# Optimization experiments

Measured on AMD Instinct MI355X. Metric: run time of the kernel, lower is better.

## Reference

```python
import jax, jax.numpy as jnp
import numpy as np
from jax import lax

B, NQ, C = 2, 1024, 2048
H, DH = 16, 128
G, CD = 4, 512          # off_grps, off_dim = C // G
LR, HR = 24, 72         # low-res grid side, high-res grid side
INTER = 64
K = LR * LR             # sampled K/V tokens (grid_size == lr_size)


def setup_inputs() -> dict:
    key = jax.random.key(0)
    ks = jax.random.split(key, 16)
    s = 0.02
    d = {}
    d['hidden_states'] = jax.random.normal(ks[0], (B, NQ, C), jnp.float32)
    d['image_hd'] = jax.random.normal(ks[1], (B, HR * HR, C), jnp.float32)
    d['wq'] = jax.random.normal(ks[2], (C, C), jnp.float32) * s
    d['wk'] = jax.random.normal(ks[3], (C, C), jnp.float32) * s
    d['wv'] = jax.random.normal(ks[4], (C, C), jnp.float32) * s
    d['wo'] = jax.random.normal(ks[5], (C, C), jnp.float32) * s
    d['conv_dw_w'] = jax.random.normal(ks[6], (CD, 1, 3, 3), jnp.float32) * s
    d['ln1_w'] = jnp.ones((CD,), jnp.float32)
    d['ln1_b'] = jnp.zeros((CD,), jnp.float32)
    d['conv_lr_proj_w'] = jax.random.normal(ks[7], (INTER, CD), jnp.float32) * s
    d['proj_int_w'] = jax.random.normal(ks[8], (INTER, CD), jnp.float32) * s
    d['proj_int_b'] = jnp.zeros((INTER,), jnp.float32)
    d['ln2_w'] = jnp.ones((INTER,), jnp.float32)
    d['ln2_b'] = jnp.zeros((INTER,), jnp.float32)
    d['conv_off_w'] = jax.random.normal(ks[9], (2, INTER), jnp.float32) * s
    d['k_hd_w'] = jax.random.normal(ks[10], (C, C), jnp.float32) * s
    d['k_hd_b'] = jnp.zeros((C,), jnp.float32)
    d['v_hd_w'] = jax.random.normal(ks[11], (C, C), jnp.float32) * s
    d['v_hd_b'] = jnp.zeros((C,), jnp.float32)
    return d


def _ln_channels(x, w, b, eps=1e-5):
    # LayerNorm2d: normalize over channel axis of [N, C, H, W]
    mu = jnp.mean(x, axis=1, keepdims=True)
    var = jnp.var(x, axis=1, keepdims=True)
    xn = (x - mu) * lax.rsqrt(var + eps)
    return xn * w[None, :, None, None] + b[None, :, None, None]


def _tokens_to_grid(x, S):
    # [B, S*S, C] -> [B*G, CD, S, S]  (group channels like einops '(b) (h w) (g c) -> (b g) c h w')
    return x.reshape(B, S, S, G, CD).transpose(0, 3, 4, 1, 2).reshape(B * G, CD, S, S)


def _bilinear_sample(img, grid):
    # img [N, C, Hh, Wh]; grid [N, K, 2] (x, y) normalized to [-1, 1], align_corners=True
    N, Cc, Hh, Wh = img.shape
    x = (grid[..., 0] + 1.0) * 0.5 * (Wh - 1)
    y = (grid[..., 1] + 1.0) * 0.5 * (Hh - 1)
    x0f, y0f = jnp.floor(x), jnp.floor(y)
    wx = (x - x0f)[:, None, :]
    wy = (y - y0f)[:, None, :]
    x0 = jnp.clip(x0f.astype(jnp.int32), 0, Wh - 1)
    x1 = jnp.clip(x0 + 1, 0, Wh - 1)
    y0 = jnp.clip(y0f.astype(jnp.int32), 0, Hh - 1)
    y1 = jnp.clip(y0 + 1, 0, Hh - 1)
    imgf = img.reshape(N, Cc, Hh * Wh)
    gather = jax.vmap(lambda im, ix: im[:, ix])  # ([C,HW],[K]) -> [C,K]
    v00 = gather(imgf, y0 * Wh + x0)
    v01 = gather(imgf, y0 * Wh + x1)
    v10 = gather(imgf, y1 * Wh + x0)
    v11 = gather(imgf, y1 * Wh + x1)
    return (v00 * (1 - wx) * (1 - wy) + v01 * wx * (1 - wy)
            + v10 * (1 - wx) * wy + v11 * wx * wy)  # [N, C, K]


def _ref_grid():
    # normalized reference points as in _grid_generate (centers / (S-1) * 2 - 1)
    yy = (jnp.linspace(0.5, LR - 0.5, LR) / (LR - 1.0)) * 2.0 - 1.0
    xx = (jnp.linspace(0.5, LR - 0.5, LR) / (LR - 1.0)) * 2.0 - 1.0
    gy, gx = jnp.meshgrid(yy, xx, indexing='ij')
    return jnp.stack([gx, gy], axis=-1).reshape(K, 2)  # (x, y)


def reference(hidden_states, image_hd, wq, wk, wv, wo, conv_dw_w, ln1_w, ln1_b,
              conv_lr_proj_w, proj_int_w, proj_int_b, ln2_w, ln2_b, conv_off_w,
              k_hd_w, k_hd_b, v_hd_w, v_hd_b):
    # ---- QKV on the full sequence ----
    q = hidden_states @ wq.T
    k_txt = hidden_states @ wk.T
    v_txt = hidden_states @ wv.T

    # ---- offset network on LR image tokens (first LR*LR tokens) ----
    lr = _tokens_to_grid(hidden_states[:, :K, :], LR)          # [B*G, CD, LR, LR]
    x = lax.conv_general_dilated(lr, conv_dw_w, (1, 1), 'SAME',
                                 feature_group_count=CD,
                                 dimension_numbers=('NCHW', 'OIHW', 'NCHW'))
    x = jax.nn.silu(x)
    x = _ln_channels(x, ln1_w, ln1_b)
    x = jnp.einsum('nchw,oc->nohw', x, conv_lr_proj_w)          # 1x1 conv -> [B*G, INTER, LR, LR]
    # intention gate from spatially pooled group features
    pooled = jnp.mean(lr, axis=(2, 3))                          # [B*G, CD]
    gate = jax.nn.sigmoid(pooled @ proj_int_w.T + proj_int_b)   # [B*G, INTER]
    x = x * gate[:, :, None, None]
    x = _ln_channels(x, ln2_w, ln2_b)
    off = jnp.einsum('nchw,oc->nohw', x, conv_off_w)            # [B*G, 2, LR, LR]
    off = off.transpose(0, 2, 3, 1).reshape(B * G, K, 2)        # (x, y)
    pos = jnp.tanh(_ref_grid()[None] + off)                     # sampling locs in [-1, 1]

    # ---- deformable gather from HD features ----
    hd = _tokens_to_grid(image_hd, HR)                          # [B*G, CD, HR, HR]
    samp = _bilinear_sample(hd, pos)                            # [B*G, CD, K]
    samp = samp.reshape(B, G, CD, K).transpose(0, 3, 1, 2).reshape(B, K, C)
    k_hd = samp @ k_hd_w.T + k_hd_b
    v_hd = samp @ v_hd_w.T + v_hd_b

    # ---- attention: causal over text tokens, HD tokens fully visible ----
    k_all = jnp.concatenate([k_txt, k_hd], axis=1)              # [B, NQ+K, C]
    v_all = jnp.concatenate([v_txt, v_hd], axis=1)
    qh = q.reshape(B, NQ, H, DH).transpose(0, 2, 1, 3)
    kh = k_all.reshape(B, NQ + K, H, DH).transpose(0, 2, 1, 3)
    vh = v_all.reshape(B, NQ + K, H, DH).transpose(0, 2, 1, 3)
    scores = jnp.einsum('bhqd,bhkd->bhqk', qh, kh) / jnp.sqrt(jnp.float32(DH))
    col = jnp.arange(NQ + K)
    row = jnp.arange(NQ)
    allow = (col[None, :] >= NQ) | (col[None, :] <= row[:, None])
    scores = jnp.where(allow[None, None], scores, jnp.float32(-1e9))
    attn = jax.nn.softmax(scores, axis=-1)
    out = jnp.einsum('bhqk,bhkd->bhqd', attn, vh)
    out = out.transpose(0, 2, 1, 3).reshape(B, NQ, C)
    return out @ wo.T
```

## Files before the change

kernel.cpp:

```cpp
#include <hip/hip_runtime.h>

typedef unsigned short u16;
typedef unsigned int u32;
typedef __attribute__((ext_vector_type(8))) short bf8;
typedef __attribute__((ext_vector_type(4))) float f4;
typedef __attribute__((ext_vector_type(4))) unsigned short us4;

constexpr int B = 2;
constexpr int NQ = 1024;
constexpr int C = 2048;
constexpr int DH = 128;
constexpr int G = 4;
constexpr int CD = 512;
constexpr int LR = 24;
constexpr int HR = 72;
constexpr int INTER = 64;
constexpr int K = LR * LR;
constexpr int NKV = NQ + K;

#define MFMA16(a, b, c) __builtin_amdgcn_mfma_f32_16x16x32_bf16(a, b, c, 0, 0, 0)
#define GLDS(g, l)                                                         \
  __builtin_amdgcn_global_load_lds(                                        \
      (const __attribute__((address_space(1))) void*)(g),                  \
      (__attribute__((address_space(3))) void*)(l), 16, 0, 0)
#define SB()                               \
  do {                                     \
    __builtin_amdgcn_sched_barrier(0);     \
    __builtin_amdgcn_s_barrier();          \
    __builtin_amdgcn_sched_barrier(0);     \
  } while (0)
#define WVM(n)                                              \
  do {                                                      \
    asm volatile("s_waitcnt vmcnt(" #n ")" ::: "memory");   \
    __builtin_amdgcn_sched_barrier(0);                      \
  } while (0)

__device__ __forceinline__ u16 f2bf1(float f) {
  u32 u = __float_as_uint(f);
  u32 r = (u + 0x7fffu + ((u >> 16) & 1u)) >> 16;
  return (u16)r;
}

__global__ __launch_bounds__(256) void f2bf_k9b(
    const float* __restrict__ s0, const float* __restrict__ s1,
    const float* __restrict__ s2, const float* __restrict__ s3,
    const float* __restrict__ s4, const float* __restrict__ s5,
    const float* __restrict__ s6, const float* __restrict__ plrw,
    const float* __restrict__ cdw, u16* __restrict__ d0, u16* __restrict__ d1,
    u16* __restrict__ d2, u16* __restrict__ d3, u16* __restrict__ d4,
    u16* __restrict__ d5, u16* __restrict__ d6, float* __restrict__ wt,
    float* __restrict__ x1, float* __restrict__ pooled) {
  __shared__ float SH[16 * 577];
  const int y = blockIdx.y;
  const int t = threadIdx.x;
  if (y == 7) {
    if (blockIdx.x >= 128) return;
    const int idx = blockIdx.x * 256 + t;
    wt[idx] = plrw[(idx & 63) * 512 + (idx >> 6)];
    return;
  }
  if (y == 8) {
    if (blockIdx.x >= 256) return;
    const int n = blockIdx.x >> 5, cg = blockIdx.x & 31;
    const int b = n >> 2, g = n & 3;
    const int c0 = cg * 16;
    {
      const int c = t & 15, pr = t >> 4;
      const float* src = s0 + (size_t)b * 1024 * 2048 + g * 512 + c0 + c;
#pragma unroll 4
      for (int j = 0; j < 36; ++j) {
        const int p = j * 16 + pr;
        SH[c * 577 + p] = src[(size_t)p * 2048];
      }
    }
    __syncthreads();
    {
      const int c = t >> 4, seg = t & 15;
      float s = 0.f;
      for (int i = 0; i < 36; ++i) s += SH[c * 577 + seg * 36 + i];
      s += __shfl_xor(s, 1);
      s += __shfl_xor(s, 2);
      s += __shfl_xor(s, 4);
      s += __shfl_xor(s, 8);
      if (seg == 0) pooled[n * 512 + c0 + c] = s * (1.f / 576.f);
    }
    const size_t base_out = (size_t)(n * 512 + c0) * 576;
    for (int j = 0; j < 36; ++j) {
      const int idx = j * 256 + t;
      const int c = idx / 576, p = idx - c * 576;
      const int yy0 = p / 24, xx0 = p - yy0 * 24;
      const float* wp = cdw + (c0 + c) * 9;
      float s = 0.f;
#pragma unroll
      for (int dy = -1; dy <= 1; ++dy)
#pragma unroll
        for (int dx = -1; dx <= 1; ++dx) {
          const int yy = yy0 + dy, xx = xx0 + dx;
          if (yy < 0 || yy >= 24 || xx < 0 || xx >= 24) continue;
          s += SH[c * 577 + yy * 24 + xx] * wp[(dy + 1) * 3 + dx + 1];
        }
      x1[base_out + idx] = s / (1.f + expf(-s));
    }
    return;
  }
  const float* s;
  u16* d;
  switch (y) {
    case 0: s = s0; d = d0; break;
    case 1: s = s1; d = d1; break;
    case 2: s = s2; d = d2; break;
    case 3: s = s3; d = d3; break;
    case 4: s = s4; d = d4; break;
    case 5: s = s5; d = d5; break;
    default: s = s6; d = d6; break;
  }
  u16* L = (u16*)SH;
  const int pc = blockIdx.x;
  const int mb = pc >> 5, kb = pc & 31;
  const int rin = t >> 2, c0 = (t & 3) * 16;
  const float* src = s + (size_t)(mb * 64 + rin) * 2048 + kb * 64 + c0;
#pragma unroll
  for (int j = 0; j < 16; j += 4) {
    float4 v = *(const float4*)(src + j);
    L[rin * 68 + c0 + j] = f2bf1(v.x);
    L[rin * 68 + c0 + j + 1] = f2bf1(v.y);
    L[rin * 68 + c0 + j + 2] = f2bf1(v.z);
    L[rin * 68 + c0 + j + 3] = f2bf1(v.w);
  }
  __syncthreads();
  u16* dst = d + (size_t)pc * 4096 + t * 16;
#pragma unroll
  for (int gg = 0; gg < 2; ++gg) {
    const int g = t * 2 + gg;
    const int rh = g & 15, ks2 = (g >> 4) & 3, kc = (g >> 6) & 1, fr = g >> 7;
    const int row = fr * 16 + rh, cc = kc * 32 + ks2 * 8;
    us4 o0, o1;
    o0.x = L[row * 68 + cc];     o0.y = L[row * 68 + cc + 1];
    o0.z = L[row * 68 + cc + 2]; o0.w = L[row * 68 + cc + 3];
    o1.x = L[row * 68 + cc + 4]; o1.y = L[row * 68 + cc + 5];
    o1.z = L[row * 68 + cc + 6]; o1.w = L[row * 68 + cc + 7];
    *(us4*)(dst + gg * 8) = o0;
    *(us4*)(dst + gg * 8 + 4) = o1;
  }
}

__global__ __launch_bounds__(512, 2) void gemm_queue(
    const u16* __restrict__ Ast, const u16* __restrict__ Wq,
    const u16* __restrict__ Wk, const u16* __restrict__ Wv,
    const u16* __restrict__ sampst, const u16* __restrict__ khwst,
    const u16* __restrict__ vhwst, const float* __restrict__ khb,
    const float* __restrict__ vhb, u16* __restrict__ outq,
    u16* __restrict__ kg, u16* __restrict__ vg, u32* __restrict__ qctr) {
  __shared__ u16 As[2][4][4096];
  __shared__ u16 Bs[2][4][4096];
  __shared__ int s_item;
  const int tid = threadIdx.x, lane = tid & 63, w = tid >> 6;
  const int ks = lane >> 4, r = lane & 15;

  while (true) {
    __syncthreads();
    if (tid == 0) s_item = (int)atomicAdd(qctr, 1u);
    __syncthreads();
    const int item = s_item;
    if (item >= 336) break;

    if (item < 192) {
      const int wm = w >> 2, wn = w & 3;
      const int swz = (item & 7) * 24 + (item >> 3);
      const int mt = swz / 24, nt = swz % 24;
      const u16* Wst = (nt < 8) ? Wq : (nt < 16) ? Wk : Wv;
      const int nb0 = (nt & 7) * 4;
      const int mb0 = mt * 4;

#define ST_A03(bi, kt)                                                        \
  do {                                                                        \
    GLDS(Ast + ((size_t)(mb0 + 0) * 32 + (kt)) * 4096 + tid * 8,              \
         &As[bi][0][tid * 8]);                                                \
    GLDS(Ast + ((size_t)(mb0 + 2) * 32 + (kt)) * 4096 + tid * 8,              \
         &As[bi][2][tid * 8]);                                                \
  } while (0)
#define ST_A47(bi, kt)                                                        \
  do {                                                                        \
    GLDS(Ast + ((size_t)(mb0 + 1) * 32 + (kt)) * 4096 + tid * 8,              \
         &As[bi][1][tid * 8]);                                                \
    GLDS(Ast + ((size_t)(mb0 + 3) * 32 + (kt)) * 4096 + tid * 8,              \
         &As[bi][3][tid * 8]);                                                \
  } while (0)
#define ST_B01(bi, kt)                                                        \
  do {                                                                        \
    GLDS(Wst + ((size_t)(nb0 + 0) * 32 + (kt)) * 4096 + tid * 8,              \
         &Bs[bi][0][tid * 8]);                                                \
    GLDS(Wst + ((size_t)(nb0 + 1) * 32 + (kt)) * 4096 + tid * 8,              \
         &Bs[bi][1][tid * 8]);                                                \
  } while (0)
#define ST_B23(bi, kt)                                                        \
  do {                                                                        \
    GLDS(Wst + ((size_t)(nb0 + 2) * 32 + (kt)) * 4096 + tid * 8,              \
         &Bs[bi][2][tid * 8]);                                                \
    GLDS(Wst + ((size_t)(nb0 + 3) * 32 + (kt)) * 4096 + tid * 8,              \
         &Bs[bi][3][tid * 8]);                                                \
  } while (0)
#define RD_A(dst, bi, half, kc)                                               \
  _Pragma("unroll") for (int i2 = 0; i2 < 4; ++i2) dst[i2] =                  \
      *(const bf8*)(&As[bi][wm * 2 + (half)]                                  \
                       [((i2 * 2 + (kc)) * 4 + ks) * 128 + r * 8]);
#define RD_B(dst, bi, kc)                                                     \
  _Pragma("unroll") for (int j2 = 0; j2 < 4; ++j2) dst[j2] =                  \
      *(const bf8*)(&Bs[bi][wn][((j2 * 2 + (kc)) * 4 + ks) * 128 + r * 8]);
#define MM(ACC, AF, BF)                                                       \
  do {                                                                        \
    __builtin_amdgcn_s_setprio(1);                                            \
    _Pragma("unroll") for (int i3 = 0; i3 < 4; ++i3)                          \
        _Pragma("unroll") for (int j3 = 0; j3 < 4; ++j3) ACC[i3][j3] =        \
            MFMA16(AF[i3], BF[j3], ACC[i3][j3]);                              \
    __builtin_amdgcn_s_setprio(0);                                            \
  } while (0)

      f4 accA[4][4], accB[4][4];
#pragma unroll
      for (int i = 0; i < 4; ++i)
#pragma unroll
        for (int j = 0; j < 4; ++j) {
          accA[i][j] = f4{0.f, 0.f, 0.f, 0.f};
          accB[i][j] = f4{0.f, 0.f, 0.f, 0.f};
        }
      bf8 af[4], b0[4], b1[4];

      ST_A03(0, 0); ST_B01(0, 0); ST_B23(0, 0); ST_A47(0, 0);
      ST_A03(1, 1); ST_B01(1, 1);
      WVM(6);
      SB();

      for (int t = 0; t < 32; ++t) {
        const int buf = t & 1;
        RD_A(af, buf, 0, 0);
        RD_B(b0, buf, 0);
        if (t + 1 < 32) ST_B23(buf ^ 1, t + 1);
        SB();
        MM(accA, af, b0);
        SB();
        RD_A(af, buf, 0, 1);
        RD_B(b1, buf, 1);
        if (t + 1 < 32) ST_A47(buf ^ 1, t + 1);
        SB();
        MM(accA, af, b1);
        if (t + 1 < 32) { WVM(8); } else { WVM(0); }
        SB();
        RD_A(af, buf, 1, 0);
        if (t + 2 < 32) ST_A03(buf, t + 2);
        SB();
        MM(accB, af, b0);
        SB();
        RD_A(af, buf, 1, 1);
        if (t + 2 < 32) ST_B01(buf, t + 2);
        SB();
        MM(accB, af, b1);
        if (t + 2 < 32) { WVM(6); } else if (t + 1 < 32) { WVM(2); }
        SB();
      }

#define EPI(ACC, HALF)                                                        \
  _Pragma("unroll") for (int i = 0; i < 4; ++i)                               \
      _Pragma("unroll") for (int j = 0; j < 4; ++j)                           \
          _Pragma("unroll") for (int rr = 0; rr < 4; ++rr) {                  \
    const int m = mt * 256 + wm * 128 + (HALF)*64 + i * 16 + ks * 4 + rr;     \
    const int n = nt * 256 + wn * 64 + j * 16 + r;                            \
    const float v = ACC[i][j][rr];                                            \
    const int sel = n >> 11, nn = n & 2047, hh = nn >> 7, dd = nn & 127;      \
    const int bb = m >> 10, qq = m & 1023;                                    \
    const u16 bv = f2bf1(v);                                                  \
    if (sel == 0) {                                                           \
      outq[(size_t)m * 2048 + nn] = bv;                                       \
    } else if (sel == 1) {                                                    \
      kg[(((size_t)(bb * 16 + hh) * 50 + (qq >> 5)) * 16 + (dd >> 3)) * 256 + \
         (qq & 31) * 8 + (dd & 7)] = bv;                                      \
    } else {                                                                  \
      vg[((size_t)(bb * 16 + hh) * 200 + (qq >> 3)) * 1024 + dd * 8 +         \
         (qq & 7)] = bv;                                                      \
    }                                                                         \
  }
      EPI(accA, 0)
      EPI(accB, 1)
#undef EPI
    } else {
      u16* A3 = &As[0][0][0];
      u16* Bk3 = &As[0][0][0] + 12288;
      u16* Bv3 = &Bs[0][0][0];
      const int hb = item - 192;
      const int mt = hb / 16, nt = hb % 16;
      const int ma0 = mt * 2, nb0 = nt * 2;
      const bool is_v = (w >= 4);
      const int wv4 = w & 3;
      const int wr = wv4 >> 1, wc = wv4 & 1;
      const u16* Wsrc = is_v ? vhwst : khwst;
      u16* Wdst = is_v ? Bv3 : Bk3;
      const u16* Brd = is_v ? Bv3 : Bk3;

#define HDST(bi, kt)                                                          \
  do {                                                                        \
    const int kb_ = (kt) >> 1, kc_ = (kt) & 1;                                \
    GLDS(sampst + ((size_t)(ma0 + (w >> 2)) * 32 + kb_) * 4096 +              \
             (w & 3) * 1024 + kc_ * 512 + lane * 8,                           \
         &A3[(bi)*4096 + w * 512 + lane * 8]);                                \
    _Pragma("unroll") for (int r2 = 0; r2 < 2; ++r2) {                        \
      const int run = r2 * 4 + wv4;                                           \
      GLDS(Wsrc + ((size_t)(nb0 + (run >> 2)) * 32 + kb_) * 4096 +            \
               (run & 3) * 1024 + kc_ * 512 + lane * 8,                       \
           &Wdst[(bi)*4096 + run * 512 + lane * 8]);                          \
    }                                                                         \
  } while (0)

      f4 acc[4][4];
#pragma unroll
      for (int i = 0; i < 4; ++i)
#pragma unroll
        for (int j = 0; j < 4; ++j) acc[i][j] = f4{0.f, 0.f, 0.f, 0.f};

      HDST(0, 0);
      HDST(1, 1);
      int rd = 0;
      for (int kt = 0; kt < 64; ++kt) {
        SB();
        if (kt + 2 < 64) {
          const int wb = (rd + 2 >= 3) ? rd - 1 : rd + 2;
          HDST(wb, kt + 2);
          WVM(6);
        } else if (kt + 1 < 64) {
          WVM(3);
        } else {
          WVM(0);
        }
        SB();
        bf8 af2[4], bw[4];
#pragma unroll
        for (int i = 0; i < 4; ++i)
          af2[i] = *(const bf8*)(&A3[rd * 4096 + (wr * 4 + i) * 512 +
                                     ks * 128 + r * 8]);
#pragma unroll
        for (int j = 0; j < 4; ++j)
          bw[j] = *(const bf8*)(&Brd[rd * 4096 + (wc * 4 + j) * 512 +
                                     ks * 128 + r * 8]);
        __builtin_amdgcn_s_setprio(1);
#pragma unroll
        for (int i = 0; i < 4; ++i)
#pragma unroll
          for (int j = 0; j < 4; ++j)
            acc[i][j] = MFMA16(af2[i], bw[j], acc[i][j]);
        __builtin_amdgcn_s_setprio(0);
        rd = (rd + 1 >= 3) ? 0 : rd + 1;
      }
#undef HDST
      const int rbase = ks * 4;
      const float* bias = is_v ? vhb : khb;
#pragma unroll
      for (int i = 0; i < 4; ++i)
#pragma unroll
        for (int j = 0; j < 4; ++j) {
          const int nn = nt * 128 + wc * 64 + j * 16 + r;
          const int hh = nn >> 7, dd = nn & 127;
#pragma unroll
          for (int rr = 0; rr < 4; ++rr) {
            const int m = mt * 128 + wr * 64 + i * 16 + rbase + rr;
            const int bb = m / 576;
            const int kv = 1024 + (m - bb * 576);
            const u16 bv = f2bf1(acc[i][j][rr] + bias[nn]);
            if (!is_v) {
              kg[(((size_t)(bb * 16 + hh) * 50 + (kv >> 5)) * 16 + (dd >> 3)) *
                     256 +
                 (kv & 31) * 8 + (dd & 7)] = bv;
            } else {
              vg[((size_t)(bb * 16 + hh) * 200 + (kv >> 3)) * 1024 + dd * 8 +
                 (kv & 7)] = bv;
            }
          }
        }
    }
  }
}

__global__ __launch_bounds__(256) void gemm_out3(const u16* __restrict__ Ast,
                                                 const u16* __restrict__ W0,
                                                 float* __restrict__ outf) {
  __shared__ u16 As[3][4096];
  __shared__ u16 Bs[3][4096];
  const int tid = threadIdx.x, lane = tid & 63, w = tid >> 6;
  const int wr = w >> 1, wc = w & 1;
  const int ksl = lane >> 4, rl = lane & 15;
  const int xcd = blockIdx.x & 7, idx = blockIdx.x >> 3;
  const int mt = (xcd >> 2) * 8 + idx / 4;
  const int nt = (xcd & 3) * 4 + idx % 4;
  const u16* Wp = W0;
  const int ma0 = mt * 2;
  const int nb0 = nt * 2;

#define GST2(dstArr, srcBase, tb0, kt)                                     \
  do {                                                                     \
    const int kb_ = (kt) >> 1, kc_ = (kt) & 1;                             \
    _Pragma("unroll") for (int r2 = 0; r2 < 2; ++r2) {                     \
      const int run = r2 * 4 + w;                                          \
      GLDS(srcBase + ((size_t)((tb0) + (run >> 2)) * 32 + kb_) * 4096 +    \
               (run & 3) * 1024 + kc_ * 512 + lane * 8,                    \
           &dstArr[run * 512 + lane * 8]);                                 \
    }                                                                      \
  } while (0)

  f4 acc[4][4];
#pragma unroll
  for (int i = 0; i < 4; ++i)
#pragma unroll
    for (int j = 0; j < 4; ++j) acc[i][j] = f4{0.f, 0.f, 0.f, 0.f};

  GST2(As[0], Ast, ma0, 0);
  GST2(Bs[0], Wp, nb0, 0);
  GST2(As[1], Ast, ma0, 1);
  GST2(Bs[1], Wp, nb0, 1);
  int rd = 0;
  for (int kt = 0; kt < 64; ++kt) {
    SB();
    if (kt + 2 < 64) {
      const int wb = (rd + 2 >= 3) ? rd - 1 : rd + 2;
      GST2(As[wb], Ast, ma0, kt + 2);
      GST2(Bs[wb], Wp, nb0, kt + 2);
      WVM(8);
    } else if (kt + 1 < 64) {
      WVM(4);
    } else {
      WVM(0);
    }
    SB();
    bf8 af[4], bw[4];
#pragma unroll
    for (int i = 0; i < 4; ++i)
      af[i] = *(const bf8*)(&As[rd][(wr * 4 + i) * 512 + ksl * 128 + rl * 8]);
#pragma unroll
    for (int j = 0; j < 4; ++j)
      bw[j] = *(const bf8*)(&Bs[rd][(wc * 4 + j) * 512 + ksl * 128 + rl * 8]);
    __builtin_amdgcn_s_setprio(1);
#pragma unroll
    for (int i = 0; i < 4; ++i)
#pragma unroll
      for (int j = 0; j < 4; ++j)
        acc[i][j] = MFMA16(af[i], bw[j], acc[i][j]);
    __builtin_amdgcn_s_setprio(0);
    rd = (rd + 1 >= 3) ? 0 : rd + 1;
  }
#undef GST2

  const int rbase = ksl * 4;
#pragma unroll
  for (int i = 0; i < 4; ++i)
#pragma unroll
    for (int j = 0; j < 4; ++j) {
      const int n = nt * 128 + wc * 64 + j * 16 + rl;
#pragma unroll
      for (int rr = 0; rr < 4; ++rr) {
        const int m = mt * 128 + wr * 64 + i * 16 + rbase + rr;
        outf[(size_t)m * 2048 + n] = acc[i][j][rr];
      }
    }
}

__global__ __launch_bounds__(256) void lnproj_gate(
    const float* __restrict__ x1, const float* __restrict__ ln1w,
    const float* __restrict__ ln1b, const float* __restrict__ wt,
    const float* __restrict__ pooled, const float* __restrict__ piw,
    const float* __restrict__ pib, float* __restrict__ x2,
    float* __restrict__ gate) {
  __shared__ float Xs[512][68];
  __shared__ float rs[4][64], rss[4][64];
  const int bidx = blockIdx.x;
  const int t = threadIdx.x;
  if (bidx >= 72) {
    const int idx = (bidx - 72) * 256 + t;
    const int n = idx >> 6, o = idx & 63;
    const float* pb = pooled + n * 512;
    const float* wb = piw + o * 512;
    float s = pib[o];
    for (int c = 0; c < 512; ++c) s += pb[c] * wb[c];
    gate[idx] = 1.f / (1.f + expf(-s));
    return;
  }
  const int n = bidx / 9, pc = bidx % 9;
  const int p0 = pc * 64;
  {
    const int pl = t & 63, c4 = t >> 6;
    const float* src = x1 + (size_t)n * 512 * 576 + p0 + pl;
#pragma unroll 4
    for (int j = 0; j < 128; ++j) {
      const int c = j * 4 + c4;
      Xs[c][pl] = src[(size_t)c * 576];
    }
  }
  __syncthreads();
  {
    const int pl = t & 63, q = t >> 6;
    float s = 0.f, ss = 0.f;
    for (int c = q * 128; c < q * 128 + 128; ++c) {
      const float v = Xs[c][pl];
      s += v;
      ss += v * v;
    }
    rs[q][pl] = s;
    rss[q][pl] = ss;
    __syncthreads();
    const float S = rs[0][pl] + rs[1][pl] + rs[2][pl] + rs[3][pl];
    const float SS = rss[0][pl] + rss[1][pl] + rss[2][pl] + rss[3][pl];
    const float mean = S * (1.f / 512.f);
    const float inv = rsqrtf(SS * (1.f / 512.f) - mean * mean + 1e-5f);
    for (int c = q * 128; c < q * 128 + 128; ++c)
      Xs[c][pl] = (Xs[c][pl] - mean) * inv * ln1w[c] + ln1b[c];
  }
  __syncthreads();
  {
    const int o4 = (t & 15) * 4, pl0 = (t >> 4) * 4;
    float acc[4][4] = {};
    for (int c = 0; c < 512; ++c) {
      const f4 xv = *(const f4*)(&Xs[c][pl0]);
      const f4 wv = *(const f4*)(&wt[c * 64 + o4]);
#pragma unroll
      for (int i = 0; i < 4; ++i)
#pragma unroll
        for (int j = 0; j < 4; ++j) acc[i][j] += wv[i] * xv[j];
    }
#pragma unroll
    for (int i = 0; i < 4; ++i) {
      f4 ov;
      ov[0] = acc[i][0]; ov[1] = acc[i][1];
      ov[2] = acc[i][2]; ov[3] = acc[i][3];
      *(f4*)(&x2[(size_t)(n * 64 + o4 + i) * 576 + p0 + pl0]) = ov;
    }
  }
}

__global__ __launch_bounds__(256) void pos_sample(
    const float* __restrict__ x2, const float* __restrict__ gate,
    const float* __restrict__ ln2w, const float* __restrict__ ln2b,
    const float* __restrict__ offw, const float* __restrict__ img,
    u16* __restrict__ sampst) {
  const int bk = blockIdx.x;
  const int b = bk / K, k = bk % K;
  __shared__ int s_idx[G][4];
  __shared__ float s_w[G][4];
  const int t = threadIdx.x;
  const int g = t >> 6, lane = t & 63;
  {
    const int n = b * G + g;
    float v = x2[((size_t)n * INTER + lane) * K + k] * gate[n * INTER + lane];
    float s = v, ss = v * v;
    for (int o = 32; o; o >>= 1) {
      s += __shfl_xor(s, o);
      ss += __shfl_xor(ss, o);
    }
    const float mean = s * (1.f / INTER);
    const float var = ss * (1.f / INTER) - mean * mean;
    const float xn = (v - mean) * rsqrtf(var + 1e-5f) * ln2w[lane] + ln2b[lane];
    float ox = xn * offw[lane];
    float oy = xn * offw[INTER + lane];
    for (int o = 32; o; o >>= 1) {
      ox += __shfl_xor(ox, o);
      oy += __shfl_xor(oy, o);
    }
    if (lane == 0) {
      const int yi = k / LR, xi = k % LR;
      const float rx = (xi + 0.5f) / 23.f * 2.f - 1.f;
      const float ry = (yi + 0.5f) / 23.f * 2.f - 1.f;
      const float px = tanhf(rx + ox), py = tanhf(ry + oy);
      const float x = (px + 1.f) * 0.5f * (HR - 1);
      const float y = (py + 1.f) * 0.5f * (HR - 1);
      const float x0f = floorf(x), y0f = floorf(y);
      const float wx = x - x0f, wy = y - y0f;
      const int x0 = min(max((int)x0f, 0), HR - 1);
      const int x1 = min(x0 + 1, HR - 1);
      const int y0 = min(max((int)y0f, 0), HR - 1);
      const int y1 = min(y0 + 1, HR - 1);
      s_idx[g][0] = y0 * HR + x0;
      s_idx[g][1] = y0 * HR + x1;
      s_idx[g][2] = y1 * HR + x0;
      s_idx[g][3] = y1 * HR + x1;
      s_w[g][0] = (1.f - wx) * (1.f - wy);
      s_w[g][1] = wx * (1.f - wy);
      s_w[g][2] = (1.f - wx) * wy;
      s_w[g][3] = wx * wy;
    }
  }
  __syncthreads();
  const int m = b * 576 + k;
  const int mb = m >> 6, fr = (m >> 4) & 3, r = m & 15;
  const int ch0 = t * 8;
  const int gg = ch0 >> 9;
  const float* ib = img + (size_t)b * HR * HR * C + ch0;
  float v[8];
#pragma unroll
  for (int j = 0; j < 8; ++j) v[j] = 0.f;
#pragma unroll
  for (int q = 0; q < 4; ++q) {
    const float wq_ = s_w[gg][q];
    const float* p = ib + (size_t)s_idx[gg][q] * C;
    const float4 a = *(const float4*)p;
    const float4 c = *(const float4*)(p + 4);
    v[0] += wq_ * a.x; v[1] += wq_ * a.y; v[2] += wq_ * a.z; v[3] += wq_ * a.w;
    v[4] += wq_ * c.x; v[5] += wq_ * c.y; v[6] += wq_ * c.z; v[7] += wq_ * c.w;
  }
  const int kb = ch0 >> 6, kc = (ch0 >> 5) & 1, ks3 = (ch0 >> 3) & 3;
  u16* dst = sampst + ((size_t)(mb * 32 + kb)) * 4096 +
             (((fr * 2 + kc) * 4 + ks3) * 16 + r) * 8;
  us4 o0, o1;
  o0.x = f2bf1(v[0]); o0.y = f2bf1(v[1]); o0.z = f2bf1(v[2]); o0.w = f2bf1(v[3]);
  o1.x = f2bf1(v[4]); o1.y = f2bf1(v[5]); o1.z = f2bf1(v[6]); o1.w = f2bf1(v[7]);
  *(us4*)dst = o0;
  *(us4*)(dst + 4) = o1;
}

__global__ __launch_bounds__(256) void attn_u64(
    const u16* __restrict__ qb, const u16* __restrict__ kg,
    const u16* __restrict__ vg, u16* __restrict__ aob_st) {
  const int i = blockIdx.x;
  const int pair = i & 255, half = i >> 8;
  const int bh = pair & 31;
  const int q8 = pair >> 5;
  const int qblk = half ? (15 - q8) : q8;
  const int b = bh >> 4, h = bh & 15;
  const int q0 = qblk * 64;
  const int tid = threadIdx.x, lane = tid & 63, w = tid >> 6;
  const int qw = q0 + w * 16;
  const int col = lane & 15, kpart = lane >> 4, rbase = kpart * 4;
  __shared__ u16 Ks[2][8192];
  __shared__ u16 Vs[2][8192];
  __shared__ u16 Pl[4][16 * 72];
  bf8 qf[4];
  {
    const u16* qp =
        qb + (size_t)(b * 1024 + qw + col) * 2048 + h * 128 + kpart * 8;
#pragma unroll
    for (int dc = 0; dc < 4; ++dc) qf[dc] = *(const bf8*)(qp + dc * 32);
  }
  f4 o[8];
#pragma unroll
  for (int df = 0; df < 8; ++df) o[df] = f4{0.f, 0.f, 0.f, 0.f};
  float m_r[4] = {-1e30f, -1e30f, -1e30f, -1e30f};
  float l_p[4] = {0.f, 0.f, 0.f, 0.f};
  const float scale = 0.08838834764831845f;
  const int nt_text = qblk + 1;
  const int nt = nt_text + 9;
  const u16* kbh = kg + (size_t)bh * (NKV * 128);
  const u16* vbh = vg + (size_t)bh * (NKV * 128);
  u16* pw = &Pl[w][0];

#define ASTG64(bi, kv0)                                                       \
  do {                                                                        \
    const u16* gk = kbh + (size_t)((kv0) >> 5) * 4096 + w * 2048 + lane * 8;  \
    GLDS(gk, &Ks[bi][w * 2048 + lane * 8]);                                   \
    GLDS(gk + 512, &Ks[bi][w * 2048 + 512 + lane * 8]);                       \
    GLDS(gk + 1024, &Ks[bi][w * 2048 + 1024 + lane * 8]);                     \
    GLDS(gk + 1536, &Ks[bi][w * 2048 + 1536 + lane * 8]);                     \
    const u16* gv = vbh + (size_t)((kv0) >> 3) * 1024 + w * 2048 + lane * 8;  \
    GLDS(gv, &Vs[bi][w * 2048 + lane * 8]);                                   \
    GLDS(gv + 512, &Vs[bi][w * 2048 + 512 + lane * 8]);                       \
    GLDS(gv + 1024, &Vs[bi][w * 2048 + 1024 + lane * 8]);                     \
    GLDS(gv + 1536, &Vs[bi][w * 2048 + 1536 + lane * 8]);                     \
  } while (0)

  ASTG64(0, 0);
  int cur = 0;
  for (int t = 0; t < nt; ++t) {
    const bool is_text = t < nt_text;
    const int kv0 = is_text ? (t << 6) : (1024 + ((t - nt_text) << 6));
    SB();
    if (t + 1 < nt) {
      const int t1 = t + 1;
      const int kv1 =
          (t1 < nt_text) ? (t1 << 6) : (1024 + ((t1 - nt_text) << 6));
      ASTG64(cur ^ 1, kv1);
      WVM(8);
    } else {
      WVM(0);
    }
    SB();
    const u16* ksb = &Ks[cur][0];
    const u16* vsb = &Vs[cur][0];
    f4 s0 = {0.f, 0.f, 0.f, 0.f}, s1 = {0.f, 0.f, 0.f, 0.f};
    f4 s2 = {0.f, 0.f, 0.f, 0.f}, s3 = {0.f, 0.f, 0.f, 0.f};
    __builtin_amdgcn_s_setprio(1);
#pragma unroll
    for (int dc = 0; dc < 4; ++dc) {
      const int dblk = dc * 4 + kpart;
      bf8 k0f = *(const bf8*)(ksb + (dblk * 32 + col) * 8);
      bf8 k1f = *(const bf8*)(ksb + (dblk * 32 + 16 + col) * 8);
      bf8 k2f = *(const bf8*)(ksb + 4096 + (dblk * 32 + col) * 8);
      bf8 k3f = *(const bf8*)(ksb + 4096 + (dblk * 32 + 16 + col) * 8);
      s0 = MFMA16(qf[dc], k0f, s0);
      s1 = MFMA16(qf[dc], k1f, s1);
      s2 = MFMA16(qf[dc], k2f, s2);
      s3 = MFMA16(qf[dc], k3f, s3);
    }
    __builtin_amdgcn_s_setprio(0);
    float sa[4][4], loc[4], p[4][4];
    bool grow = false;
    const bool need_mask = is_text && (kv0 + 63 > qw);
#pragma unroll
    for (int rr = 0; rr < 4; ++rr) {
      float a0 = s0[rr] * scale, a1 = s1[rr] * scale;
      float a2 = s2[rr] * scale, a3 = s3[rr] * scale;
      if (need_mask) {
        const int qg = qw + rbase + rr;
        if (kv0 + col > qg) a0 = -1e30f;
        if (kv0 + 16 + col > qg) a1 = -1e30f;
        if (kv0 + 32 + col > qg) a2 = -1e30f;
        if (kv0 + 48 + col > qg) a3 = -1e30f;
      }
      sa[rr][0] = a0; sa[rr][1] = a1; sa[rr][2] = a2; sa[rr][3] = a3;
      loc[rr] = fmaxf(fmaxf(a0, a1), fmaxf(a2, a3));
      grow |= (loc[rr] > m_r[rr] + 8.f);
    }
    if (__any(grow)) {
      float fr[4];
#pragma unroll
      for (int rr = 0; rr < 4; ++rr) {
        float mx = loc[rr];
        mx = fmaxf(mx, __shfl_xor(mx, 1));
        mx = fmaxf(mx, __shfl_xor(mx, 2));
        mx = fmaxf(mx, __shfl_xor(mx, 4));
        mx = fmaxf(mx, __shfl_xor(mx, 8));
        const float mn = fmaxf(m_r[rr], mx);
        fr[rr] = __expf(m_r[rr] - mn);
        m_r[rr] = mn;
#pragma unroll
        for (int jj = 0; jj < 4; ++jj) p[rr][jj] = __expf(sa[rr][jj] - mn);
        l_p[rr] = l_p[rr] * fr[rr] + p[rr][0] + p[rr][1] + p[rr][2] + p[rr][3];
      }
#pragma unroll
      for (int df = 0; df < 8; ++df) {
        o[df][0] *= fr[0]; o[df][1] *= fr[1];
        o[df][2] *= fr[2]; o[df][3] *= fr[3];
      }
    } else {
#pragma unroll
      for (int rr = 0; rr < 4; ++rr) {
#pragma unroll
        for (int jj = 0; jj < 4; ++jj) p[rr][jj] = __expf(sa[rr][jj] - m_r[rr]);
        l_p[rr] += p[rr][0] + p[rr][1] + p[rr][2] + p[rr][3];
      }
    }
#pragma unroll
    for (int rr = 0; rr < 4; ++rr) {
      pw[(rbase + rr) * 72 + col] = f2bf1(p[rr][0]);
      pw[(rbase + rr) * 72 + 16 + col] = f2bf1(p[rr][1]);
      pw[(rbase + rr) * 72 + 32 + col] = f2bf1(p[rr][2]);
      pw[(rbase + rr) * 72 + 48 + col] = f2bf1(p[rr][3]);
    }
    bf8 pa0 = *(const bf8*)(pw + col * 72 + kpart * 8);
    bf8 pa1 = *(const bf8*)(pw + col * 72 + 32 + kpart * 8);
    __builtin_amdgcn_s_setprio(1);
#pragma unroll
    for (int df = 0; df < 8; ++df) {
      bf8 vf0 = *(const bf8*)(vsb + (kpart * 128 + df * 16 + col) * 8);
      bf8 vf1 = *(const bf8*)(vsb + ((kpart + 4) * 128 + df * 16 + col) * 8);
      o[df] = MFMA16(pa0, vf0, o[df]);
      o[df] = MFMA16(pa1, vf1, o[df]);
    }
    __builtin_amdgcn_s_setprio(0);
    cur ^= 1;
  }
#undef ASTG64
  float inv[4];
#pragma unroll
  for (int rr = 0; rr < 4; ++rr) {
    float ps = l_p[rr];
    ps += __shfl_xor(ps, 1);
    ps += __shfl_xor(ps, 2);
    ps += __shfl_xor(ps, 4);
    ps += __shfl_xor(ps, 8);
    inv[rr] = 1.f / ps;
  }
#pragma unroll
  for (int rr = 0; rr < 4; ++rr) {
    const int m = b * 1024 + qw + rbase + rr;
    const int mb = m >> 6, fr3 = (m >> 4) & 3, r16 = m & 15;
#pragma unroll
    for (int df = 0; df < 8; ++df) {
      const int ncol = h * 128 + df * 16 + col;
      const int kb = ncol >> 6, kc = (ncol >> 5) & 1, ks3 = (ncol >> 3) & 3,
                j0 = ncol & 7;
      aob_st[((size_t)(mb * 32 + kb)) * 4096 +
             (((fr3 * 2 + kc) * 4 + ks3) * 16 + r16) * 8 + j0] =
          f2bf1(o[df][rr] * inv[rr]);
    }
  }
}

extern "C" void kernel_launch(void* const* d_in, const int* in_sizes, int n_in,
                              void* d_out, int out_size, void* d_ws,
                              size_t ws_size, hipStream_t stream) {
  const float* hs = (const float*)d_in[0];
  const float* img = (const float*)d_in[1];
  const float* wq = (const float*)d_in[2];
  const float* wk = (const float*)d_in[3];
  const float* wv = (const float*)d_in[4];
  const float* wo = (const float*)d_in[5];
  const float* cdw = (const float*)d_in[6];
  const float* ln1w = (const float*)d_in[7];
  const float* ln1b = (const float*)d_in[8];
  const float* plrw = (const float*)d_in[9];
  const float* piw = (const float*)d_in[10];
  const float* pib = (const float*)d_in[11];
  const float* ln2w = (const float*)d_in[12];
  const float* ln2b = (const float*)d_in[13];
  const float* offw = (const float*)d_in[14];
  const float* khw = (const float*)d_in[15];
  const float* khb = (const float*)d_in[16];
  const float* vhw = (const float*)d_in[17];
  const float* vhb = (const float*)d_in[18];
  float* outp = (float*)d_out;

  u16* wsp = (u16*)d_ws;
  const size_t SZ = 4194304;
  u16* hs_st = wsp;
  u16* wq_st = wsp + SZ;
  u16* wk_st = wsp + 2 * SZ;
  u16* wv_st = wsp + 3 * SZ;
  u16* wo_st = wsp + 4 * SZ;
  u16* khw_st = wsp + 5 * SZ;
  u16* vhw_st = wsp + 6 * SZ;
  u16* qb_bf = wsp + 7 * SZ;
  u16* samp_st = wsp + 8 * SZ;
  u16* kg = wsp + 8 * SZ + 2359296;
  u16* vg = kg + 6553600;
  float* x1b = (float*)kg + 2359296;
  float* x2b = x1b + 2359296;
  float* poolb = x2b + 294912;
  float* gb = poolb + 4096;
  float* wtb = (float*)(vg + 6553600);
  u32* qctr = (u32*)(wtb + 32768);
  u16* aob_st = wq_st;

  dim3 blk(256);
  f2bf_k9b<<<dim3(1024, 9), blk, 0, stream>>>(
      hs, wq, wk, wv, wo, khw, vhw, plrw, cdw, hs_st, wq_st, wk_st, wv_st,
      wo_st, khw_st, vhw_st, wtb, x1b, poolb);
  lnproj_gate<<<dim3(74), blk, 0, stream>>>(x1b, ln1w, ln1b, wtb, poolb, piw,
                                            pib, x2b, gb);
  pos_sample<<<dim3(B * K), blk, 0, stream>>>(x2b, gb, ln2w, ln2b, offw, img,
                                              samp_st);
  hipMemsetAsync(qctr, 0, 4, stream);
  gemm_queue<<<dim3(256), dim3(512), 0, stream>>>(
      hs_st, wq_st, wk_st, wv_st, samp_st, khw_st, vhw_st, khb, vhb, qb_bf,
      kg, vg, qctr);
  attn_u64<<<dim3(512), blk, 0, stream>>>(qb_bf, kg, vg, aob_st);
  gemm_out3<<<dim3(256), blk, 0, stream>>>(aob_st, wo_st, outp);
}
```

Before: 330.7 us.

## Split fused K/V HD projection tiles into separate work-queue items

The high-res K/V projection items in the persistent GEMM queue previously computed both K and V for one 128x128 tile, with half the warps on each. They are now split into separate K and V items (144 each, queue grows from 336 to 480), so all 8 warps cooperate on one output with a 4x2 MFMA arrangement per warp. This gives more, smaller items for better load balance across CUs. In exchange, the sampled A tile is loaded twice (once per K and once per V item), and there is more queue and sync overhead per item.

```diff
diff --git a/kernel.cpp b/kernel.cpp
--- a/kernel.cpp
+++ b/kernel.cpp
@@ -162,7 +162,7 @@
     if (tid == 0) s_item = (int)atomicAdd(qctr, 1u);
     __syncthreads();
     const int item = s_item;
-    if (item >= 336) break;
+    if (item >= 480) break;
 
     if (item < 192) {
       const int wm = w >> 2, wn = w & 3;
@@ -284,79 +284,73 @@
 #undef EPI
     } else {
       u16* A3 = &As[0][0][0];
-      u16* Bk3 = &As[0][0][0] + 12288;
-      u16* Bv3 = &Bs[0][0][0];
-      const int hb = item - 192;
+      u16* B3 = &Bs[0][0][0];
+      const int htile = item - 192;
+      const bool is_v = (htile >= 144);
+      const int hb = is_v ? (htile - 144) : htile;
       const int mt = hb / 16, nt = hb % 16;
       const int ma0 = mt * 2, nb0 = nt * 2;
-      const bool is_v = (w >= 4);
-      const int wv4 = w & 3;
-      const int wr = wv4 >> 1, wc = wv4 & 1;
+      const int wr = w >> 2, wc = w & 3;
       const u16* Wsrc = is_v ? vhwst : khwst;
-      u16* Wdst = is_v ? Bv3 : Bk3;
-      const u16* Brd = is_v ? Bv3 : Bk3;
-
-#define HDST(bi, kt)                                                          \
+
+#define HDS1(bi, kt)                                                          \
   do {                                                                        \
     const int kb_ = (kt) >> 1, kc_ = (kt) & 1;                                \
     GLDS(sampst + ((size_t)(ma0 + (w >> 2)) * 32 + kb_) * 4096 +              \
              (w & 3) * 1024 + kc_ * 512 + lane * 8,                           \
          &A3[(bi)*4096 + w * 512 + lane * 8]);                                \
-    _Pragma("unroll") for (int r2 = 0; r2 < 2; ++r2) {                        \
-      const int run = r2 * 4 + wv4;                                           \
-      GLDS(Wsrc + ((size_t)(nb0 + (run >> 2)) * 32 + kb_) * 4096 +            \
-               (run & 3) * 1024 + kc_ * 512 + lane * 8,                       \
-           &Wdst[(bi)*4096 + run * 512 + lane * 8]);                          \
-    }                                                                         \
-  } while (0)
-
-      f4 acc[4][4];
+    GLDS(Wsrc + ((size_t)(nb0 + (w >> 2)) * 32 + kb_) * 4096 +                \
+             (w & 3) * 1024 + kc_ * 512 + lane * 8,                           \
+         &B3[(bi)*4096 + w * 512 + lane * 8]);                                \
+  } while (0)
+
+      f4 acc[4][2];
 #pragma unroll
       for (int i = 0; i < 4; ++i)
 #pragma unroll
-        for (int j = 0; j < 4; ++j) acc[i][j] = f4{0.f, 0.f, 0.f, 0.f};
-
-      HDST(0, 0);
-      HDST(1, 1);
+        for (int j = 0; j < 2; ++j) acc[i][j] = f4{0.f, 0.f, 0.f, 0.f};
+
+      HDS1(0, 0);
+      HDS1(1, 1);
       int rd = 0;
       for (int kt = 0; kt < 64; ++kt) {
         SB();
         if (kt + 2 < 64) {
           const int wb = (rd + 2 >= 3) ? rd - 1 : rd + 2;
-          HDST(wb, kt + 2);
-          WVM(6);
+          HDS1(wb, kt + 2);
+          WVM(4);
         } else if (kt + 1 < 64) {
-          WVM(3);
+          WVM(2);
         } else {
           WVM(0);
         }
         SB();
-        bf8 af2[4], bw[4];
+        bf8 af2[4], bw[2];
 #pragma unroll
         for (int i = 0; i < 4; ++i)
           af2[i] = *(const bf8*)(&A3[rd * 4096 + (wr * 4 + i) * 512 +
                                      ks * 128 + r * 8]);
 #pragma unroll
-        for (int j = 0; j < 4; ++j)
-          bw[j] = *(const bf8*)(&Brd[rd * 4096 + (wc * 4 + j) * 512 +
-                                     ks * 128 + r * 8]);
+        for (int j = 0; j < 2; ++j)
+          bw[j] = *(const bf8*)(&B3[rd * 4096 + (wc * 2 + j) * 512 +
+                                    ks * 128 + r * 8]);
         __builtin_amdgcn_s_setprio(1);
 #pragma unroll
         for (int i = 0; i < 4; ++i)
 #pragma unroll
-          for (int j = 0; j < 4; ++j)
+          for (int j = 0; j < 2; ++j)
             acc[i][j] = MFMA16(af2[i], bw[j], acc[i][j]);
         __builtin_amdgcn_s_setprio(0);
         rd = (rd + 1 >= 3) ? 0 : rd + 1;
       }
-#undef HDST
+#undef HDS1
       const int rbase = ks * 4;
       const float* bias = is_v ? vhb : khb;
 #pragma unroll
       for (int i = 0; i < 4; ++i)
 #pragma unroll
-        for (int j = 0; j < 4; ++j) {
-          const int nn = nt * 128 + wc * 64 + j * 16 + r;
+        for (int j = 0; j < 2; ++j) {
+          const int nn = nt * 128 + (wc * 2 + j) * 16 + r;
           const int hh = nn >> 7, dd = nn & 127;
 #pragma unroll
           for (int rr = 0; rr < 4; ++rr) {
```

Result: faster. 320.7 us (-3.0%).
